# Kernel optimization log

Hardware: AMD Instinct MI355X
Metric: run time of the kernel (lower is better)

The kernel has to match this reference:

```python
import jax, jax.numpy as jnp
import numpy as np
import math

B = 8192       # batch (tokens)
HID = 4096     # hidden size
H = 32         # num query heads
KV = 8         # num kv heads
GQA = H // KV  # 4
D = 128        # head dim
RBIT = 128     # hash bits
QKV = (H + 2 * KV) * D  # 6144


def setup_inputs() -> dict:
    key = jax.random.key(0)
    k1, k2, k3 = jax.random.split(key, 3)
    hidden = jax.random.normal(k1, (B, HID), jnp.float32)
    proj_w = jax.random.normal(k2, (HID, QKV), jnp.float32) * 0.02
    proj_b = jnp.zeros((QKV,), jnp.float32)
    # xavier_uniform init for hash weight [D, RBIT]
    limit = math.sqrt(6.0 / (D + RBIT))
    hash_w = jax.random.uniform(k3, (D, RBIT), jnp.float32, -limit, limit)
    return {"hidden": hidden, "proj_w": proj_w, "proj_b": proj_b, "hash_w": hash_w}


def reference(hidden, proj_w, proj_b, hash_w):
    # fused qkv projection
    qkv = hidden @ proj_w + proj_b                     # [B, QKV]
    q = qkv[:, : H * D].reshape(B, H, D)               # [B, H, D]
    k = qkv[:, H * D : (H + KV) * D].reshape(B, KV, 1, D)
    k = jnp.broadcast_to(k, (B, KV, GQA, D)).reshape(B, H, D)  # GQA expand

    inv_sqrt_d = 1.0 / math.sqrt(D)
    attn_weights = jnp.einsum("bhd,bhd->bh", q, k) * inv_sqrt_d  # with_norm=True

    # hash codes: BinaryStochastic (training mode): (tanh(x)+1)/2
    q_code = (jnp.tanh(q @ hash_w) + 1.0) * 0.5        # [B, H, RBIT]
    k_code = (jnp.tanh(k @ hash_w) + 1.0) * 0.5
    ham_dist = jnp.abs(q_code - k_code).sum(axis=-1)   # [B, H]
    ham_weights = 1.0 - 2.0 * ham_dist / RBIT

    # with_norm: scale by |q| |k| / sqrt(D)
    q_norm = jnp.linalg.norm(q, axis=-1)
    k_norm = jnp.linalg.norm(k, axis=-1)
    ham_weights = ham_weights * q_norm * k_norm * inv_sqrt_d

    return attn_weights.reshape(-1), ham_weights.reshape(-1)
```

## Files before the change

### kernel.cpp

```cpp
#include <hip/hip_runtime.h>
#include <hip/hip_bf16.h>
#include <cstdint>
#include <cstddef>

#define B_TOK 8192
#define HID   4096
#define NH    32
#define NKV   8
#define DH    128
#define RB    128
#define KDIM  4096
#define NOUT  5120
#define QKVW  6144

typedef __bf16 bf16x8 __attribute__((ext_vector_type(8)));
typedef __bf16 bf16x4 __attribute__((ext_vector_type(4)));
typedef float  f32x4  __attribute__((ext_vector_type(4)));

__device__ __forceinline__ void async_ld16(const void* g, void* l) {
  __builtin_amdgcn_global_load_lds(
      (__attribute__((address_space(1))) void*)(g),
      (__attribute__((address_space(3))) void*)(l), 16, 0, 0);
}

__device__ __forceinline__ float code_of(float x) {
  const float e = exp2f(x * -2.885390081777927f);
  return __builtin_amdgcn_rcpf(1.0f + e);
}


#define NB_HID  16384
#define NB_WT   5120
#define NB_HASH 64

__global__ void prep_kernel(const float* __restrict__ hidden, __bf16* __restrict__ Abf,
                            const float* __restrict__ W, __bf16* __restrict__ Wt,
                            const float* __restrict__ hw, __bf16* __restrict__ hwT) {
  __shared__ float t[64][65];
  const int bx  = blockIdx.x;
  const int tid = threadIdx.x;

  if (bx < NB_HID) {
    const int i = bx * 256 + tid;
    const float4 v0 = ((const float4*)hidden)[2 * i];
    const float4 v1 = ((const float4*)hidden)[2 * i + 1];
    bf16x8 o;
    o[0] = (__bf16)v0.x; o[1] = (__bf16)v0.y; o[2] = (__bf16)v0.z; o[3] = (__bf16)v0.w;
    o[4] = (__bf16)v1.x; o[5] = (__bf16)v1.y; o[6] = (__bf16)v1.z; o[7] = (__bf16)v1.w;
    ((bf16x8*)Abf)[i] = o;
  } else if (bx < NB_HID + NB_WT) {
    const int bt = bx - NB_HID;
    const int n0 = (bt % 80) * 64;
    const int k0 = (bt / 80) * 64;
    const int c4 = tid & 15;
    const int rr = tid >> 4;
#pragma unroll
    for (int j = 0; j < 4; ++j) {
      const int r = rr + j * 16;
      const float4 v = *(const float4*)&W[(size_t)(k0 + r) * QKVW + n0 + c4 * 4];
      t[r][c4 * 4 + 0] = v.x; t[r][c4 * 4 + 1] = v.y;
      t[r][c4 * 4 + 2] = v.z; t[r][c4 * 4 + 3] = v.w;
    }
    __syncthreads();
    const int c8 = tid & 7;
    const int nn = tid >> 3;
#pragma unroll
    for (int jj = 0; jj < 2; ++jj) {
      const int n = nn + jj * 32;
      bf16x8 o;
#pragma unroll
      for (int i = 0; i < 8; ++i) o[i] = (__bf16)t[c8 * 8 + i][n];
      *(bf16x8*)&Wt[(size_t)(n0 + n) * KDIM + k0 + c8 * 8] = o;
    }
  } else {
    const int idx = (bx - NB_HID - NB_WT) * 256 + tid;
    const int r = idx >> 7;
    const int d = idx & 127;
    hwT[r * RB + d] = (__bf16)hw[(size_t)d * RB + r];
  }
}


__global__ void gemm_qk(const __bf16* __restrict__ A,
                        const __bf16* __restrict__ Bt,
                        const float* __restrict__ bias,
                        __bf16* __restrict__ C) {
  __shared__ __bf16 As[2][128 * 32];
  __shared__ __bf16 Bs[2][128 * 32];

  const int tid  = threadIdx.x;
  const int lane = tid & 63;
  const int wave = tid >> 6;

  const int lin = blockIdx.y * 40 + blockIdx.x;
  const int xcd = lin & 7;
  const int seq = lin >> 3;
  const int n0 = (xcd * 5 + (seq % 5)) * 128;
  const int m0 = (seq / 5) * 128;

  const int waveM = (wave >> 1) * 64;
  const int waveN = (wave & 1) * 64;

  const int srow  = lane >> 2;
  const int selem = (lane & 3) * 8;

  const __bf16* ga0 = A + (size_t)(m0 + wave * 16 + srow) * KDIM + selem;
  const __bf16* ga1 = ga0 + (size_t)64 * KDIM;
  const __bf16* gb0 = Bt + (size_t)(n0 + wave * 16 + srow) * KDIM + selem;
  const __bf16* gb1 = gb0 + (size_t)64 * KDIM;
  __bf16* la0 = &As[0][wave * 512];
  __bf16* la1 = &As[0][(wave + 4) * 512];
  __bf16* lb0 = &Bs[0][wave * 512];
  __bf16* lb1 = &Bs[0][(wave + 4) * 512];
  __bf16* la0b = &As[1][wave * 512];
  __bf16* la1b = &As[1][(wave + 4) * 512];
  __bf16* lb0b = &Bs[1][wave * 512];
  __bf16* lb1b = &Bs[1][(wave + 4) * 512];

  const int fr = lane & 15;
  const int fk = (lane >> 4) * 8;

  f32x4 acc[4][4] = {};

  for (int kt = 0; kt < KDIM / 64; ++kt) {
    const int k0 = kt * 64;
    async_ld16(ga0 + k0, la0);  async_ld16(ga0 + k0 + 32, la0b);
    async_ld16(ga1 + k0, la1);  async_ld16(ga1 + k0 + 32, la1b);
    async_ld16(gb0 + k0, lb0);  async_ld16(gb0 + k0 + 32, lb0b);
    async_ld16(gb1 + k0, lb1);  async_ld16(gb1 + k0 + 32, lb1b);
    __syncthreads();

#pragma unroll
    for (int ks = 0; ks < 2; ++ks) {
      bf16x8 af[4], bfr[4];
#pragma unroll
      for (int mi = 0; mi < 4; ++mi)
        af[mi] = *(const bf16x8*)(&As[ks][(waveM + mi * 16 + fr) * 32 + fk]);
#pragma unroll
      for (int ni = 0; ni < 4; ++ni)
        bfr[ni] = *(const bf16x8*)(&Bs[ks][(waveN + ni * 16 + fr) * 32 + fk]);
#pragma unroll
      for (int mi = 0; mi < 4; ++mi)
#pragma unroll
        for (int ni = 0; ni < 4; ++ni)
          acc[mi][ni] = __builtin_amdgcn_mfma_f32_16x16x32_bf16(af[mi], bfr[ni],
                                                                acc[mi][ni], 0, 0, 0);
    }
    __syncthreads();
  }

  const int cl = lane & 15;
  const int rq = (lane >> 4) * 4;
#pragma unroll
  for (int ni = 0; ni < 4; ++ni) {
    const int gn = n0 + waveN + ni * 16 + cl;
    const float bb = bias[gn];
#pragma unroll
    for (int mi = 0; mi < 4; ++mi) {
      const int gm = m0 + waveM + mi * 16 + rq;
#pragma unroll
      for (int r = 0; r < 4; ++r)
        C[(size_t)(gm + r) * NOUT + gn] = (__bf16)(acc[mi][ni][r] + bb);
    }
  }
}


__global__ void phase2_kernel(const __bf16* __restrict__ QK,
                              const __bf16* __restrict__ hwT,
                              float* __restrict__ out) {
  __shared__ __bf16 As[48][136];
  __shared__ float code[40][132];
  __shared__ float rednorm[40];
  __shared__ float reddot[32];

  const int tid  = threadIdx.x;
  const int lane = tid & 63;
  const int wave = tid >> 6;
  const int b = blockIdx.x;

  const __bf16* src = QK + (size_t)b * NOUT;
  for (int i = tid; i < 640; i += 256) {
    const int row = i >> 4;
    const int col = (i & 15) * 8;
    *(uint4*)(&As[row][col]) = *(const uint4*)(src + i * 8);
  }

  const int fr = lane & 15;
  const int fk = (lane >> 4) * 8;
  bf16x8 bf[2][4];
#pragma unroll
  for (int nn = 0; nn < 2; ++nn) {
    const int ni = wave + nn * 4;
#pragma unroll
    for (int ks = 0; ks < 4; ++ks)
      bf[nn][ks] = *(const bf16x8*)(hwT + (size_t)(ni * 16 + fr) * RB + ks * 32 + fk);
  }
  __syncthreads();

#pragma unroll
  for (int mi = 0; mi < 3; ++mi) {
    bf16x8 af[4];
#pragma unroll
    for (int ks = 0; ks < 4; ++ks)
      af[ks] = *(const bf16x8*)(&As[mi * 16 + fr][ks * 32 + fk]);
#pragma unroll
    for (int nn = 0; nn < 2; ++nn) {
      const int ni = wave + nn * 4;
      f32x4 acc = {0.f, 0.f, 0.f, 0.f};
#pragma unroll
      for (int ks = 0; ks < 4; ++ks)
        acc = __builtin_amdgcn_mfma_f32_16x16x32_bf16(af[ks], bf[nn][ks], acc, 0, 0, 0);
      const int row0 = mi * 16 + (lane >> 4) * 4;
      const int col  = ni * 16 + (lane & 15);
#pragma unroll
      for (int r = 0; r < 4; ++r) {
        const int row = row0 + r;
        if (row < 40) code[row][col] = code_of(acc[r]);
      }
    }
  }

  {
    const int q = lane >> 4;
    const int c = lane & 15;
    const int ti = (wave == 1 || wave == 3) ? 1 : 0;
    const int tj = (wave >= 2) ? 2 : ti;
    bf16x8 fa[4], fb[4];
#pragma unroll
    for (int ks = 0; ks < 4; ++ks) {
      fa[ks] = *(const bf16x8*)(&As[ti * 16 + fr][ks * 32 + fk]);
      fb[ks] = *(const bf16x8*)(&As[tj * 16 + fr][ks * 32 + fk]);
    }
    f32x4 g = {0.f, 0.f, 0.f, 0.f};
#pragma unroll
    for (int ks = 0; ks < 4; ++ks)
      g = __builtin_amdgcn_mfma_f32_16x16x32_bf16(fa[ks], fb[ks], g, 0, 0, 0);
    if (ti == tj) {
      if ((c >> 2) == q) rednorm[ti * 16 + c] = g[c & 3];
    } else {
      if (c == ti * 4 + q) {
#pragma unroll
        for (int r = 0; r < 4; ++r) reddot[ti * 16 + q * 4 + r] = g[r];
      }
    }
    if (wave == 0) {
      bf16x8 fc[4];
#pragma unroll
      for (int ks = 0; ks < 4; ++ks)
        fc[ks] = *(const bf16x8*)(&As[32 + fr][ks * 32 + fk]);
      f32x4 g2 = {0.f, 0.f, 0.f, 0.f};
#pragma unroll
      for (int ks = 0; ks < 4; ++ks)
        g2 = __builtin_amdgcn_mfma_f32_16x16x32_bf16(fc[ks], fc[ks], g2, 0, 0, 0);
      if ((c >> 2) == q && c < 8) rednorm[32 + c] = g2[c & 3];
    }
  }
  __syncthreads();

  const int h   = tid >> 3;
  const int sub = tid & 7;
  const int kr  = 32 + (h >> 2);
  float s = 0.f;
#pragma unroll
  for (int j = 0; j < 16; ++j) {
    const int c = sub + 8 * j;
    s += fabsf(code[h][c] - code[kr][c]);
  }
  s += __shfl_down(s, 4, 8);
  s += __shfl_down(s, 2, 8);
  s += __shfl_down(s, 1, 8);
  if (sub == 0) {
    const float invsq = 0.08838834764831843f;
    out[(size_t)b * NH + h] = reddot[h] * invsq;
    const float hamw = (1.0f - s * (1.0f / 64.0f)) *
                       sqrtf(rednorm[h]) * sqrtf(rednorm[kr]) * invsq;
    out[(size_t)(B_TOK * NH) + (size_t)b * NH + h] = hamw;
  }
}


extern "C" void kernel_launch(void* const* d_in, const int* in_sizes, int n_in,
                              void* d_out, int out_size, void* d_ws, size_t ws_size,
                              hipStream_t stream) {
  const float* hidden = (const float*)d_in[0];
  const float* proj_w = (const float*)d_in[1];
  const float* proj_b = (const float*)d_in[2];
  const float* hash_w = (const float*)d_in[3];
  float* out = (float*)d_out;

  char* w = (char*)d_ws;
  __bf16* Abf = (__bf16*)(w);
  __bf16* Wt  = (__bf16*)(w + 67108864);
  __bf16* QK  = (__bf16*)(w + 67108864 + 41943040);
  __bf16* hwT = (__bf16*)(w + 67108864 + 41943040 + 83886080);

  prep_kernel<<<NB_HID + NB_WT + NB_HASH, 256, 0, stream>>>(hidden, Abf, proj_w, Wt,
                                                            hash_w, hwT);
  gemm_qk<<<dim3(NOUT / 128, B_TOK / 128), 256, 0, stream>>>(Abf, Wt, proj_b, QK);
  phase2_kernel<<<B_TOK, 256, 0, stream>>>(QK, hwT, out);
}
```

Measured before the change: 636.3 us.

## Rewrite QK GEMM with 128x256 tiles, triple-buffered async loads, swizzled LDS

Result: faster. 608.3 us (-4.4%).

```diff
diff --git a/kernel.cpp b/kernel.cpp
--- a/kernel.cpp
+++ b/kernel.cpp
@@ -81,83 +81,102 @@
 }
 
 
-__global__ void gemm_qk(const __bf16* __restrict__ A,
-                        const __bf16* __restrict__ Bt,
-                        const float* __restrict__ bias,
-                        __bf16* __restrict__ C) {
-  __shared__ __bf16 As[2][128 * 32];
-  __shared__ __bf16 Bs[2][128 * 32];
+#define BK    32
+#define KT    (KDIM / BK)
+#define SLOT  24576
+
+__global__ __launch_bounds__(256, 2) void gemm_qk(const __bf16* __restrict__ A,
+                                                  const __bf16* __restrict__ Bt,
+                                                  const float* __restrict__ bias,
+                                                  __bf16* __restrict__ C) {
+  __shared__ __align__(1024) char smem[3 * SLOT];
 
   const int tid  = threadIdx.x;
   const int lane = tid & 63;
   const int wave = tid >> 6;
-
-  const int lin = blockIdx.y * 40 + blockIdx.x;
+  const int wm   = wave >> 1;
+  const int wn   = wave & 1;
+
+  const int lin = blockIdx.x;
   const int xcd = lin & 7;
   const int seq = lin >> 3;
-  const int n0 = (xcd * 5 + (seq % 5)) * 128;
-  const int m0 = (seq / 5) * 128;
-
-  const int waveM = (wave >> 1) * 64;
-  const int waveN = (wave & 1) * 64;
-
-  const int srow  = lane >> 2;
-  const int selem = (lane & 3) * 8;
-
-  const __bf16* ga0 = A + (size_t)(m0 + wave * 16 + srow) * KDIM + selem;
-  const __bf16* ga1 = ga0 + (size_t)64 * KDIM;
-  const __bf16* gb0 = Bt + (size_t)(n0 + wave * 16 + srow) * KDIM + selem;
-  const __bf16* gb1 = gb0 + (size_t)64 * KDIM;
-  __bf16* la0 = &As[0][wave * 512];
-  __bf16* la1 = &As[0][(wave + 4) * 512];
-  __bf16* lb0 = &Bs[0][wave * 512];
-  __bf16* lb1 = &Bs[0][(wave + 4) * 512];
-  __bf16* la0b = &As[1][wave * 512];
-  __bf16* la1b = &As[1][(wave + 4) * 512];
-  __bf16* lb0b = &Bs[1][wave * 512];
-  __bf16* lb1b = &Bs[1][(wave + 4) * 512];
+  const int m0  = (xcd * 8 + (seq & 7)) * 128;
+  const int n0  = (seq >> 3) * 256;
+
+  const int srow = tid >> 2;
+  const int sxk  = ((tid & 3) ^ ((tid >> 3) & 3)) * 8;
+  const __bf16* ga = A  + (size_t)(m0 + srow) * KDIM + sxk;
+  const __bf16* gb = Bt + (size_t)(n0 + srow) * KDIM + sxk;
+  const int ldsA = wave * 1024;
+
+#define STAGE(koff, sl) do {                                        \
+    const __bf16* ga_ = ga + (koff);                                \
+    const __bf16* gb_ = gb + (koff);                                \
+    async_ld16(ga_,              (sl) + ldsA);                      \
+    async_ld16(ga_ +  64 * KDIM, (sl) + 4096  + ldsA);              \
+    async_ld16(gb_,              (sl) + 8192  + ldsA);              \
+    async_ld16(gb_ +  64 * KDIM, (sl) + 12288 + ldsA);              \
+    async_ld16(gb_ + 128 * KDIM, (sl) + 16384 + ldsA);              \
+    async_ld16(gb_ + 192 * KDIM, (sl) + 20480 + ldsA);              \
+  } while (0)
 
   const int fr = lane & 15;
-  const int fk = (lane >> 4) * 8;
-
-  f32x4 acc[4][4] = {};
-
-  for (int kt = 0; kt < KDIM / 64; ++kt) {
-    const int k0 = kt * 64;
-    async_ld16(ga0 + k0, la0);  async_ld16(ga0 + k0 + 32, la0b);
-    async_ld16(ga1 + k0, la1);  async_ld16(ga1 + k0 + 32, la1b);
-    async_ld16(gb0 + k0, lb0);  async_ld16(gb0 + k0 + 32, lb0b);
-    async_ld16(gb1 + k0, lb1);  async_ld16(gb1 + k0 + 32, lb1b);
-    __syncthreads();
-
-#pragma unroll
-    for (int ks = 0; ks < 2; ++ks) {
-      bf16x8 af[4], bfr[4];
-#pragma unroll
-      for (int mi = 0; mi < 4; ++mi)
-        af[mi] = *(const bf16x8*)(&As[ks][(waveM + mi * 16 + fr) * 32 + fk]);
-#pragma unroll
-      for (int ni = 0; ni < 4; ++ni)
-        bfr[ni] = *(const bf16x8*)(&Bs[ks][(waveN + ni * 16 + fr) * 32 + fk]);
-#pragma unroll
-      for (int mi = 0; mi < 4; ++mi)
-#pragma unroll
-        for (int ni = 0; ni < 4; ++ni)
-          acc[mi][ni] = __builtin_amdgcn_mfma_f32_16x16x32_bf16(af[mi], bfr[ni],
-                                                                acc[mi][ni], 0, 0, 0);
-    }
-    __syncthreads();
-  }
+  const int xc = (lane >> 4) ^ ((fr >> 1) & 3);
+  const int aoff = (wm * 64 + fr) * 64 + xc * 16;
+  const int boff = (wn * 128 + fr) * 64 + xc * 16;
+
+  f32x4 acc[4][8] = {};
+
+#define COMPUTE(sl) do {                                                          \
+    bf16x8 af[4]; bf16x8 bfv[8];                                                  \
+    _Pragma("unroll")                                                             \
+    for (int mi = 0; mi < 4; ++mi)                                                \
+      af[mi] = *(const bf16x8*)((sl) + aoff + mi * 1024);                         \
+    _Pragma("unroll")                                                             \
+    for (int ni = 0; ni < 8; ++ni)                                                \
+      bfv[ni] = *(const bf16x8*)((sl) + 8192 + boff + ni * 1024);                 \
+    __builtin_amdgcn_s_setprio(1);                                                \
+    _Pragma("unroll")                                                             \
+    for (int mi = 0; mi < 4; ++mi)                                                \
+      _Pragma("unroll")                                                           \
+      for (int ni = 0; ni < 8; ++ni)                                              \
+        acc[mi][ni] = __builtin_amdgcn_mfma_f32_16x16x32_bf16(af[mi], bfv[ni],    \
+                                                              acc[mi][ni], 0, 0, 0); \
+    __builtin_amdgcn_s_setprio(0);                                                \
+  } while (0)
+
+  char* s0 = smem;
+  char* s1 = smem + SLOT;
+  char* s2 = smem + 2 * SLOT;
+
+  STAGE(0, s0);
+  STAGE(BK, s1);
+
+  for (int t = 0; t < KT - 1; ++t) {
+    asm volatile("s_waitcnt vmcnt(6)" ::: "memory");
+    __builtin_amdgcn_s_barrier();
+    __builtin_amdgcn_sched_barrier(0);
+    if (t < KT - 2) STAGE((t + 2) * BK, s2);
+    COMPUTE(s0);
+    char* tmp = s0; s0 = s1; s1 = s2; s2 = tmp;
+  }
+  asm volatile("s_waitcnt vmcnt(0)" ::: "memory");
+  __builtin_amdgcn_s_barrier();
+  __builtin_amdgcn_sched_barrier(0);
+  COMPUTE(s0);
+
+#undef STAGE
+#undef COMPUTE
 
   const int cl = lane & 15;
   const int rq = (lane >> 4) * 4;
 #pragma unroll
-  for (int ni = 0; ni < 4; ++ni) {
-    const int gn = n0 + waveN + ni * 16 + cl;
+  for (int ni = 0; ni < 8; ++ni) {
+    const int gn = n0 + wn * 128 + ni * 16 + cl;
     const float bb = bias[gn];
 #pragma unroll
     for (int mi = 0; mi < 4; ++mi) {
-      const int gm = m0 + waveM + mi * 16 + rq;
+      const int gm = m0 + wm * 64 + mi * 16 + rq;
 #pragma unroll
       for (int r = 0; r < 4; ++r)
         C[(size_t)(gm + r) * NOUT + gn] = (__bf16)(acc[mi][ni][r] + bb);
@@ -297,6 +316,6 @@
 
   prep_kernel<<<NB_HID + NB_WT + NB_HASH, 256, 0, stream>>>(hidden, Abf, proj_w, Wt,
                                                             hash_w, hwT);
-  gemm_qk<<<dim3(NOUT / 128, B_TOK / 128), 256, 0, stream>>>(Abf, Wt, proj_b, QK);
+  gemm_qk<<<1280, 256, 0, stream>>>(Abf, Wt, proj_b, QK);
   phase2_kernel<<<B_TOK, 256, 0, stream>>>(QK, hwT, out);
 }
```

## Rewrite QK GEMM with 256x320 tiles, 8 waves, swizzled LDS and phased pipelining

Applied to the files above, without the earlier changes.

Result: faster. 573.5 us (-9.9%).

```diff
diff --git a/kernel.cpp b/kernel.cpp
--- a/kernel.cpp
+++ b/kernel.cpp
@@ -14,7 +14,6 @@
 #define QKVW  6144
 
 typedef __bf16 bf16x8 __attribute__((ext_vector_type(8)));
-typedef __bf16 bf16x4 __attribute__((ext_vector_type(4)));
 typedef float  f32x4  __attribute__((ext_vector_type(4)));
 
 __device__ __forceinline__ void async_ld16(const void* g, void* l) {
@@ -81,83 +80,146 @@
 }
 
 
-__global__ void gemm_qk(const __bf16* __restrict__ A,
-                        const __bf16* __restrict__ Bt,
-                        const float* __restrict__ bias,
-                        __bf16* __restrict__ C) {
-  __shared__ __bf16 As[2][128 * 32];
-  __shared__ __bf16 Bs[2][128 * 32];
+#define BKT   64
+#define NKT   (KDIM / BKT)
+#define ASZ   32768
+#define BSZ   40960
+#define SLOT2 (ASZ + BSZ)
+
+__global__ __launch_bounds__(512, 2) void gemm_qk(const __bf16* __restrict__ A,
+                                                  const __bf16* __restrict__ Bt,
+                                                  const float* __restrict__ bias,
+                                                  __bf16* __restrict__ C) {
+  __shared__ __align__(1024) char smem[2 * SLOT2];
 
   const int tid  = threadIdx.x;
   const int lane = tid & 63;
   const int wave = tid >> 6;
-
-  const int lin = blockIdx.y * 40 + blockIdx.x;
+  const int wm   = wave >> 2;
+  const int wn   = wave & 3;
+
+  const int lin = blockIdx.x;
   const int xcd = lin & 7;
   const int seq = lin >> 3;
-  const int n0 = (xcd * 5 + (seq % 5)) * 128;
-  const int m0 = (seq / 5) * 128;
-
-  const int waveM = (wave >> 1) * 64;
-  const int waveN = (wave & 1) * 64;
-
-  const int srow  = lane >> 2;
-  const int selem = (lane & 3) * 8;
-
-  const __bf16* ga0 = A + (size_t)(m0 + wave * 16 + srow) * KDIM + selem;
-  const __bf16* ga1 = ga0 + (size_t)64 * KDIM;
-  const __bf16* gb0 = Bt + (size_t)(n0 + wave * 16 + srow) * KDIM + selem;
-  const __bf16* gb1 = gb0 + (size_t)64 * KDIM;
-  __bf16* la0 = &As[0][wave * 512];
-  __bf16* la1 = &As[0][(wave + 4) * 512];
-  __bf16* lb0 = &Bs[0][wave * 512];
-  __bf16* lb1 = &Bs[0][(wave + 4) * 512];
-  __bf16* la0b = &As[1][wave * 512];
-  __bf16* la1b = &As[1][(wave + 4) * 512];
-  __bf16* lb0b = &Bs[1][wave * 512];
-  __bf16* lb1b = &Bs[1][(wave + 4) * 512];
+  const int n0  = (xcd * 2 + (seq & 1)) * 320;
+  const int m0  = (seq >> 1) * 256;
+
+  const int sxk = ((tid & 7) ^ ((tid >> 3) & 7)) * 8;
+  const __bf16* ga0 = A  + (size_t)(m0 + (tid >> 3)) * KDIM + sxk;
+  const __bf16* gb0 = Bt + (size_t)(n0 + (tid >> 3)) * KDIM + sxk;
+  const int ldsw = wave * 1024;
+
+#define STG_A(r, dst, kk) async_ld16(ga0 + (size_t)(r) * 64 * KDIM + (kk), \
+                                     (dst) + (r) * 8192 + ldsw)
+#define STG_B(r, dst, kk) async_ld16(gb0 + (size_t)(r) * 64 * KDIM + (kk), \
+                                     (dst) + ASZ + (r) * 8192 + ldsw)
 
   const int fr = lane & 15;
-  const int fk = (lane >> 4) * 8;
-
-  f32x4 acc[4][4] = {};
-
-  for (int kt = 0; kt < KDIM / 64; ++kt) {
-    const int k0 = kt * 64;
-    async_ld16(ga0 + k0, la0);  async_ld16(ga0 + k0 + 32, la0b);
-    async_ld16(ga1 + k0, la1);  async_ld16(ga1 + k0 + 32, la1b);
-    async_ld16(gb0 + k0, lb0);  async_ld16(gb0 + k0 + 32, lb0b);
-    async_ld16(gb1 + k0, lb1);  async_ld16(gb1 + k0 + 32, lb1b);
-    __syncthreads();
-
-#pragma unroll
-    for (int ks = 0; ks < 2; ++ks) {
-      bf16x8 af[4], bfr[4];
-#pragma unroll
-      for (int mi = 0; mi < 4; ++mi)
-        af[mi] = *(const bf16x8*)(&As[ks][(waveM + mi * 16 + fr) * 32 + fk]);
-#pragma unroll
-      for (int ni = 0; ni < 4; ++ni)
-        bfr[ni] = *(const bf16x8*)(&Bs[ks][(waveN + ni * 16 + fr) * 32 + fk]);
-#pragma unroll
-      for (int mi = 0; mi < 4; ++mi)
-#pragma unroll
-        for (int ni = 0; ni < 4; ++ni)
-          acc[mi][ni] = __builtin_amdgcn_mfma_f32_16x16x32_bf16(af[mi], bfr[ni],
-                                                                acc[mi][ni], 0, 0, 0);
-    }
-    __syncthreads();
-  }
+  const int hi = lane >> 4;
+  const int xk0 = ((0 * 4 + hi) ^ (fr & 7)) * 16;
+  const int xk1 = ((1 * 4 + hi) ^ (fr & 7)) * 16;
+  const int aoffb = (wm * 128 + fr) * 128;
+  const int boffb = (wn * 80 + fr) * 128;
+
+#define LD_A(mi, xk) (*(const bf16x8*)(sc + aoffb + (mi) * 2048 + (xk)))
+#define LD_B(ni, xk) (*(const bf16x8*)(sc + ASZ + boffb + (ni) * 2048 + (xk)))
+#define SB()    __builtin_amdgcn_sched_barrier(0)
+#define BAR()   __builtin_amdgcn_s_barrier()
+#define LGKM0() asm volatile("s_waitcnt lgkmcnt(0)" ::: "memory")
+
+  f32x4 acc[8][5] = {};
+  bf16x8 bf[5][2];
+
+#define PHASE_MFMA(P) do {                                                        \
+    __builtin_amdgcn_s_setprio(1);                                                \
+    _Pragma("unroll")                                                             \
+    for (int ks = 0; ks < 2; ++ks)                                                \
+      _Pragma("unroll")                                                           \
+      for (int l = 0; l < 2; ++l)                                                 \
+        _Pragma("unroll")                                                         \
+        for (int ni = 0; ni < 5; ++ni)                                            \
+          acc[2*(P)+l][ni] = __builtin_amdgcn_mfma_f32_16x16x32_bf16(             \
+              af[l][ks], bf[ni][ks], acc[2*(P)+l][ni], 0, 0, 0);                  \
+    __builtin_amdgcn_s_setprio(0);                                                \
+  } while (0)
+
+#define PHASE_READ_A(P) do {                                                      \
+    af[0][0] = LD_A(2*(P),     xk0); af[0][1] = LD_A(2*(P),     xk1);             \
+    af[1][0] = LD_A(2*(P) + 1, xk0); af[1][1] = LD_A(2*(P) + 1, xk1);             \
+  } while (0)
+
+  {
+    char* d = smem;
+#pragma unroll
+    for (int r = 0; r < 4; ++r) STG_A(r, d, 0);
+#pragma unroll
+    for (int r = 0; r < 5; ++r) STG_B(r, d, 0);
+  }
+  asm volatile("s_waitcnt vmcnt(0)" ::: "memory");
+  BAR();
+  SB();
+
+  for (int t = 0; t < NKT; ++t) {
+    const bool st = (t < NKT - 1);
+    char* sc = smem + (t & 1) * SLOT2;
+    char* sn = smem + ((t + 1) & 1) * SLOT2;
+    const int kk = (t + 1) * BKT;
+    bf16x8 af[2][2];
+
+#pragma unroll
+    for (int ni = 0; ni < 5; ++ni) {
+      bf[ni][0] = LD_B(ni, xk0);
+      bf[ni][1] = LD_B(ni, xk1);
+    }
+    PHASE_READ_A(0);
+    SB();
+    if (st) { STG_A(0, sn, kk); STG_A(1, sn, kk); STG_A(2, sn, kk); }
+    SB();
+    BAR(); LGKM0(); SB();
+    PHASE_MFMA(0);
+    SB(); BAR();
+
+    PHASE_READ_A(1);
+    SB();
+    if (st) { STG_A(3, sn, kk); STG_B(0, sn, kk); STG_B(1, sn, kk); }
+    SB();
+    BAR(); LGKM0(); SB();
+    PHASE_MFMA(1);
+    SB(); BAR();
+
+    PHASE_READ_A(2);
+    SB();
+    if (st) { STG_B(2, sn, kk); STG_B(3, sn, kk); STG_B(4, sn, kk); }
+    SB();
+    BAR(); LGKM0(); SB();
+    PHASE_MFMA(2);
+    SB(); BAR();
+
+    PHASE_READ_A(3);
+    SB();
+    BAR(); LGKM0(); SB();
+    PHASE_MFMA(3);
+    if (st) asm volatile("s_waitcnt vmcnt(0)" ::: "memory");
+    BAR();
+    SB();
+  }
+
+#undef STG_A
+#undef STG_B
+#undef LD_A
+#undef LD_B
+#undef PHASE_MFMA
+#undef PHASE_READ_A
 
   const int cl = lane & 15;
-  const int rq = (lane >> 4) * 4;
-#pragma unroll
-  for (int ni = 0; ni < 4; ++ni) {
-    const int gn = n0 + waveN + ni * 16 + cl;
+  const int rq = hi * 4;
+#pragma unroll
+  for (int ni = 0; ni < 5; ++ni) {
+    const int gn = n0 + wn * 80 + ni * 16 + cl;
     const float bb = bias[gn];
 #pragma unroll
-    for (int mi = 0; mi < 4; ++mi) {
-      const int gm = m0 + waveM + mi * 16 + rq;
+    for (int mi = 0; mi < 8; ++mi) {
+      const int gm = m0 + wm * 128 + mi * 16 + rq;
 #pragma unroll
       for (int r = 0; r < 4; ++r)
         C[(size_t)(gm + r) * NOUT + gn] = (__bf16)(acc[mi][ni][r] + bb);
@@ -297,6 +359,6 @@
 
   prep_kernel<<<NB_HID + NB_WT + NB_HASH, 256, 0, stream>>>(hidden, Abf, proj_w, Wt,
                                                             hash_w, hwT);
-  gemm_qk<<<dim3(NOUT / 128, B_TOK / 128), 256, 0, stream>>>(Abf, Wt, proj_b, QK);
+  gemm_qk<<<512, 512, 0, stream>>>(Abf, Wt, proj_b, QK);
   phase2_kernel<<<B_TOK, 256, 0, stream>>>(QK, hwT, out);
 }
```
